# Optimization experiments

Hardware: AMD Instinct MI355X
Metric: run time of the kernel (lower is better)

## Reference

```python
import jax, jax.numpy as jnp
import numpy as np

N_NODES = 100000
N_EDGES = 1000000
D = 64
N_LAYERS = 3
BATCH = 4096


def setup_inputs() -> dict:
    key = jax.random.key(0)
    ks = jax.random.split(key, 12)
    inp = {
        "embeds": jax.random.normal(ks[0], (N_NODES, D), dtype=jnp.float32) * 0.1,
        "edge_weight": jax.random.uniform(ks[1], (N_EDGES,), dtype=jnp.float32),
        "W_gc": jax.random.normal(ks[2], (N_LAYERS, D, D), dtype=jnp.float32) * 0.1,
        "b_gc": jax.random.normal(ks[3], (N_LAYERS, 1, D), dtype=jnp.float32) * 0.1,
        "W_bi": jax.random.normal(ks[4], (N_LAYERS, D, D), dtype=jnp.float32) * 0.1,
        "b_bi": jax.random.normal(ks[5], (N_LAYERS, 1, D), dtype=jnp.float32) * 0.1,
        "edge_index": jax.random.randint(ks[6], (2, N_EDGES), 0, N_NODES, dtype=jnp.int64) if jax.config.jax_enable_x64 else jax.random.randint(ks[6], (2, N_EDGES), 0, N_NODES, dtype=jnp.int32),
        "users": jax.random.randint(ks[7], (BATCH,), 0, 50000, dtype=jnp.int32),
        "pos_items": jax.random.randint(ks[8], (BATCH,), 0, N_NODES, dtype=jnp.int32),
        "neg_items": jax.random.randint(ks[9], (BATCH,), 0, N_NODES, dtype=jnp.int32),
    }
    return inp


def _l2_normalize(x, eps=1e-12):
    # matches torch F.normalize(p=2, dim=1): divide by clamped norm
    n = jnp.sqrt(jnp.sum(x * x, axis=1, keepdims=True))
    return x / jnp.maximum(n, eps)


def reference(embeds, edge_weight, W_gc, b_gc, W_bi, b_bi, edge_index, users, pos_items, neg_items):
    row, col = edge_index[0], edge_index[1]
    n_nodes = embeds.shape[0]
    ego = embeds
    all_embeddings = [ego]
    for k in range(W_gc.shape[0]):
        # gather-scale-scatter graph aggregation
        msgs = ego[row] * edge_weight[:, None]                     # [E, D]
        side = jax.ops.segment_sum(msgs, col, num_segments=n_nodes)  # [N, D]
        sum_emb = side @ W_gc[k] + b_gc[k]                          # [N, D]
        bi_emb = (ego * side) @ W_bi[k] + b_bi[k]                   # [N, D]
        ego = jax.nn.leaky_relu(sum_emb + bi_emb, negative_slope=0.2)
        all_embeddings.append(_l2_normalize(ego))
    all_embeddings = jnp.concatenate(all_embeddings, axis=1)        # [N, 4*D]
    user_embs = all_embeddings[users]
    pos_item_embs = all_embeddings[pos_items]
    neg_item_embs = all_embeddings[neg_items]
    return (user_embs, pos_item_embs, neg_item_embs, user_embs, pos_item_embs, neg_item_embs)
```

## Files before the change

kernel.cpp:

```cpp
#include <hip/hip_runtime.h>

#define NN 100000
#define NE 1000000
#define DD 64
#define NB 4096
#define TILE 1024
#define NTILE ((NN + TILE - 1) / TILE)

__global__ __launch_bounds__(256) void k_count(
    const int* __restrict__ ei, int* __restrict__ base)
{
  const int stride = gridDim.x * blockDim.x;
  for (int e = blockIdx.x * blockDim.x + threadIdx.x; e < NE; e += stride)
    atomicAdd(&base[ei[NE + e]], 1);
}

__global__ __launch_bounds__(256) void k_scan_part(
    const int* __restrict__ base, int* __restrict__ tilesum)
{
  __shared__ int s[256];
  const int t = threadIdx.x;
  const int i0 = blockIdx.x * TILE + t * 4;
  int4 v = make_int4(0, 0, 0, 0);
  if (i0 < NN) v = *reinterpret_cast<const int4*>(base + i0);
  s[t] = v.x + v.y + v.z + v.w;
  __syncthreads();
#pragma unroll
  for (int off = 128; off >= 1; off >>= 1) {
    if (t < off) s[t] += s[t + off];
    __syncthreads();
  }
  if (t == 0) tilesum[blockIdx.x] = s[0];
}

__global__ __launch_bounds__(128) void k_scan_tiles(
    const int* __restrict__ tilesum, int* __restrict__ tileoff)
{
  __shared__ int s[128];
  const int t = threadIdx.x;
  const int v = (t < NTILE) ? tilesum[t] : 0;
  s[t] = v;
  __syncthreads();
#pragma unroll
  for (int off = 1; off < 128; off <<= 1) {
    const int u = (t >= off) ? s[t - off] : 0;
    __syncthreads();
    s[t] += u;
    __syncthreads();
  }
  if (t < NTILE) tileoff[t] = s[t] - v;
}

__global__ __launch_bounds__(256) void k_scan_apply(
    int* __restrict__ base, int* __restrict__ cursor,
    const int* __restrict__ tileoff)
{
  __shared__ int s[256];
  const int t = threadIdx.x;
  const int i0 = blockIdx.x * TILE + t * 4;
  int4 v = make_int4(0, 0, 0, 0);
  if (i0 < NN) v = *reinterpret_cast<const int4*>(base + i0);
  const int sum = v.x + v.y + v.z + v.w;
  s[t] = sum;
  __syncthreads();
#pragma unroll
  for (int off = 1; off < 256; off <<= 1) {
    const int u = (t >= off) ? s[t - off] : 0;
    __syncthreads();
    s[t] += u;
    __syncthreads();
  }
  int p = s[t] - sum + tileoff[blockIdx.x];
  if (i0 < NN) {
    const int4 o = make_int4(p, p + v.x, p + v.x + v.y, p + v.x + v.y + v.z);
    *reinterpret_cast<int4*>(base + i0) = o;
    *reinterpret_cast<int4*>(cursor + i0) = o;
  }
  if (blockIdx.x == 0 && t == 0) base[NN] = NE;
}

__global__ __launch_bounds__(256) void k_permute(
    const int* __restrict__ ei, const float* __restrict__ ew,
    int* __restrict__ cursor, int2* __restrict__ edata)
{
  const int stride = gridDim.x * blockDim.x;
  for (int e = blockIdx.x * blockDim.x + threadIdx.x; e < NE; e += stride) {
    const int c = ei[NE + e];
    const int slot = atomicAdd(&cursor[c], 1);
    edata[slot] = make_int2(ei[e], __float_as_int(ew[e]));
  }
}

__global__ __launch_bounds__(256) void k_aggregate(
    const float* __restrict__ ego, const int* __restrict__ base,
    const int2* __restrict__ edata, float* __restrict__ side)
{
  const int lane = threadIdx.x & 63;
  const int gw = (blockIdx.x * 256 + threadIdx.x) >> 6;
  const int nw = (gridDim.x * 256) >> 6;
  for (int n = gw; n < NN; n += nw) {
    const int lo = base[n];
    const int hi = base[n + 1];
    float acc = 0.f;
    int j = lo;
    for (; j + 1 < hi; j += 2) {
      const int2 a = edata[j];
      const int2 b = edata[j + 1];
      const float va = ego[(size_t)a.x * DD + lane];
      const float vb = ego[(size_t)b.x * DD + lane];
      acc = fmaf(va, __int_as_float(a.y), acc);
      acc = fmaf(vb, __int_as_float(b.y), acc);
    }
    if (j < hi) {
      const int2 a = edata[j];
      acc = fmaf(ego[(size_t)a.x * DD + lane], __int_as_float(a.y), acc);
    }
    side[(size_t)n * DD + lane] = acc;
  }
}

__global__ __launch_bounds__(256) void k_update(
    const float* __restrict__ side, const float* __restrict__ ego_in,
    float* __restrict__ ego_out, float* __restrict__ normed,
    const float* __restrict__ Wgc, const float* __restrict__ bgc,
    const float* __restrict__ Wbi, const float* __restrict__ bbi)
{
  const int lane = threadIdx.x & 63;
  float wg[DD], wb[DD];
#pragma unroll
  for (int j = 0; j < DD; ++j) {
    wg[j] = Wgc[j * DD + lane];
    wb[j] = Wbi[j * DD + lane];
  }
  const float bias = bgc[lane] + bbi[lane];
  const int gw = (blockIdx.x * 256 + threadIdx.x) >> 6;
  const int nw = (gridDim.x * 256) >> 6;
  for (int n = gw; n < NN; n += nw) {
    const float s = side[(size_t)n * DD + lane];
    const float e = ego_in[(size_t)n * DD + lane];
    const float p = s * e;
    float ag = 0.f, ab = 0.f;
#pragma unroll
    for (int j = 0; j < DD; ++j) {
      const float sj = __uint_as_float(__builtin_amdgcn_readlane(__float_as_uint(s), j));
      const float pj = __uint_as_float(__builtin_amdgcn_readlane(__float_as_uint(p), j));
      ag = fmaf(sj, wg[j], ag);
      ab = fmaf(pj, wb[j], ab);
    }
    float x = ag + ab + bias;
    x = (x > 0.f) ? x : 0.2f * x;
    ego_out[(size_t)n * DD + lane] = x;
    float ss = x * x;
#pragma unroll
    for (int off = 32; off >= 1; off >>= 1) ss += __shfl_xor(ss, off);
    const float nrm = fmaxf(sqrtf(ss), 1e-12f);
    normed[(size_t)n * DD + lane] = x / nrm;
  }
}

__global__ __launch_bounds__(256) void k_gather(
    const float* __restrict__ src, const int* __restrict__ users,
    const int* __restrict__ pos, const int* __restrict__ neg,
    float* __restrict__ out, int colOff)
{
  const int w = (blockIdx.x * 256 + threadIdx.x) >> 6;
  const int lane = threadIdx.x & 63;
  if (w >= 3 * NB) return;
  const int t = w / NB;
  const int i = w - t * NB;
  const int* idxp = (t == 0) ? users : ((t == 1) ? pos : neg);
  const int idx = idxp[i];
  const float v = src[(size_t)idx * DD + lane];
  const size_t o = (size_t)w * 256 + colOff + lane;
  out[o] = v;
  out[o + (size_t)3 * NB * 256] = v;
}

extern "C" void kernel_launch(void* const* d_in, const int* in_sizes, int n_in,
                              void* d_out, int out_size, void* d_ws, size_t ws_size,
                              hipStream_t stream)
{
  const float* embeds = (const float*)d_in[0];
  const float* ew     = (const float*)d_in[1];
  const float* Wgc    = (const float*)d_in[2];
  const float* bgc    = (const float*)d_in[3];
  const float* Wbi    = (const float*)d_in[4];
  const float* bbi    = (const float*)d_in[5];
  const int*   ei     = (const int*)d_in[6];
  const int*   users  = (const int*)d_in[7];
  const int*   pos    = (const int*)d_in[8];
  const int*   neg    = (const int*)d_in[9];
  float* out = (float*)d_out;

  float* side = (float*)d_ws;
  float* ego  = side + (size_t)NN * DD;
  float* norm = ego  + (size_t)NN * DD;
  int*   base   = (int*)(norm + (size_t)NN * DD);
  int*   cursor = base + (NN + 4);
  int*   tiles  = cursor + NN;
  int2*  edata  = (int2*)(tiles + 2 * ((NTILE + 1) & ~1));

  const dim3 blk(256);

  k_gather<<<dim3((3 * NB) / 4), blk, 0, stream>>>(embeds, users, pos, neg, out, 0);

  hipMemsetAsync(base, 0, (size_t)(NN + 4) * sizeof(int), stream);
  k_count<<<dim3(1024), blk, 0, stream>>>(ei, base);
  k_scan_part<<<dim3(NTILE), blk, 0, stream>>>(base, tiles);
  k_scan_tiles<<<dim3(1), dim3(128), 0, stream>>>(tiles, tiles + ((NTILE + 1) & ~1));
  k_scan_apply<<<dim3(NTILE), blk, 0, stream>>>(base, cursor, tiles + ((NTILE + 1) & ~1));
  k_permute<<<dim3(1024), blk, 0, stream>>>(ei, ew, cursor, edata);

  const float* cur = embeds;
  for (int k = 0; k < 3; ++k) {
    k_aggregate<<<dim3(4096), blk, 0, stream>>>(cur, base, edata, side);
    k_update<<<dim3(1024), blk, 0, stream>>>(
        side, cur, ego, norm,
        Wgc + (size_t)k * DD * DD, bgc + (size_t)k * DD,
        Wbi + (size_t)k * DD * DD, bbi + (size_t)k * DD);
    k_gather<<<dim3((3 * NB) / 4), blk, 0, stream>>>(norm, users, pos, neg, out,
                                                     DD * (k + 1));
    cur = ego;
  }
}
```

Baseline: 603.9 us.

## Record per-edge rank during counting to drop second atomic pass; unroll aggregation

The count kernel now saves the atomicAdd return value as each edge's rank within its destination node. The permute kernel then computes the slot as base plus rank instead of doing a second atomic on a cursor array, and the cursor array is removed. The rank buffer reuses the side workspace. The aggregate gather loop is unrolled by four to keep more loads in flight, and the grid sizes for count, permute and update are enlarged. The cost is an extra 4MB write and read of ranks in exchange for one fewer contended atomic per edge.

```diff
diff --git a/kernel.cpp b/kernel.cpp
--- a/kernel.cpp
+++ b/kernel.cpp
@@ -8,11 +8,11 @@
 #define NTILE ((NN + TILE - 1) / TILE)
 
 __global__ __launch_bounds__(256) void k_count(
-    const int* __restrict__ ei, int* __restrict__ base)
+    const int* __restrict__ ei, int* __restrict__ base, int* __restrict__ rank)
 {
   const int stride = gridDim.x * blockDim.x;
   for (int e = blockIdx.x * blockDim.x + threadIdx.x; e < NE; e += stride)
-    atomicAdd(&base[ei[NE + e]], 1);
+    rank[e] = atomicAdd(&base[ei[NE + e]], 1);
 }
 
 __global__ __launch_bounds__(256) void k_scan_part(
@@ -52,8 +52,7 @@
 }
 
 __global__ __launch_bounds__(256) void k_scan_apply(
-    int* __restrict__ base, int* __restrict__ cursor,
-    const int* __restrict__ tileoff)
+    int* __restrict__ base, const int* __restrict__ tileoff)
 {
   __shared__ int s[256];
   const int t = threadIdx.x;
@@ -74,19 +73,19 @@
   if (i0 < NN) {
     const int4 o = make_int4(p, p + v.x, p + v.x + v.y, p + v.x + v.y + v.z);
     *reinterpret_cast<int4*>(base + i0) = o;
-    *reinterpret_cast<int4*>(cursor + i0) = o;
   }
   if (blockIdx.x == 0 && t == 0) base[NN] = NE;
 }
 
 __global__ __launch_bounds__(256) void k_permute(
     const int* __restrict__ ei, const float* __restrict__ ew,
-    int* __restrict__ cursor, int2* __restrict__ edata)
+    const int* __restrict__ base, const int* __restrict__ rank,
+    int2* __restrict__ edata)
 {
   const int stride = gridDim.x * blockDim.x;
   for (int e = blockIdx.x * blockDim.x + threadIdx.x; e < NE; e += stride) {
     const int c = ei[NE + e];
-    const int slot = atomicAdd(&cursor[c], 1);
+    const int slot = base[c] + rank[e];
     edata[slot] = make_int2(ei[e], __float_as_int(ew[e]));
   }
 }
@@ -103,15 +102,21 @@
     const int hi = base[n + 1];
     float acc = 0.f;
     int j = lo;
-    for (; j + 1 < hi; j += 2) {
+    for (; j + 3 < hi; j += 4) {
       const int2 a = edata[j];
       const int2 b = edata[j + 1];
+      const int2 c = edata[j + 2];
+      const int2 d = edata[j + 3];
       const float va = ego[(size_t)a.x * DD + lane];
       const float vb = ego[(size_t)b.x * DD + lane];
+      const float vc = ego[(size_t)c.x * DD + lane];
+      const float vd = ego[(size_t)d.x * DD + lane];
       acc = fmaf(va, __int_as_float(a.y), acc);
       acc = fmaf(vb, __int_as_float(b.y), acc);
+      acc = fmaf(vc, __int_as_float(c.y), acc);
+      acc = fmaf(vd, __int_as_float(d.y), acc);
     }
-    if (j < hi) {
+    for (; j < hi; ++j) {
       const int2 a = edata[j];
       acc = fmaf(ego[(size_t)a.x * DD + lane], __int_as_float(a.y), acc);
     }
@@ -196,25 +201,25 @@
   float* ego  = side + (size_t)NN * DD;
   float* norm = ego  + (size_t)NN * DD;
   int*   base   = (int*)(norm + (size_t)NN * DD);
-  int*   cursor = base + (NN + 4);
-  int*   tiles  = cursor + NN;
+  int*   tiles  = base + (NN + 4);
   int2*  edata  = (int2*)(tiles + 2 * ((NTILE + 1) & ~1));
+  int*   rank = (int*)side;
 
   const dim3 blk(256);
 
   k_gather<<<dim3((3 * NB) / 4), blk, 0, stream>>>(embeds, users, pos, neg, out, 0);
 
   hipMemsetAsync(base, 0, (size_t)(NN + 4) * sizeof(int), stream);
-  k_count<<<dim3(1024), blk, 0, stream>>>(ei, base);
+  k_count<<<dim3(4096), blk, 0, stream>>>(ei, base, rank);
   k_scan_part<<<dim3(NTILE), blk, 0, stream>>>(base, tiles);
   k_scan_tiles<<<dim3(1), dim3(128), 0, stream>>>(tiles, tiles + ((NTILE + 1) & ~1));
-  k_scan_apply<<<dim3(NTILE), blk, 0, stream>>>(base, cursor, tiles + ((NTILE + 1) & ~1));
-  k_permute<<<dim3(1024), blk, 0, stream>>>(ei, ew, cursor, edata);
+  k_scan_apply<<<dim3(NTILE), blk, 0, stream>>>(base, tiles + ((NTILE + 1) & ~1));
+  k_permute<<<dim3(4096), blk, 0, stream>>>(ei, ew, base, rank, edata);
 
   const float* cur = embeds;
   for (int k = 0; k < 3; ++k) {
     k_aggregate<<<dim3(4096), blk, 0, stream>>>(cur, base, edata, side);
-    k_update<<<dim3(1024), blk, 0, stream>>>(
+    k_update<<<dim3(2048), blk, 0, stream>>>(
         side, cur, ego, norm,
         Wgc + (size_t)k * DD * DD, bgc + (size_t)k * DD,
         Wbi + (size_t)k * DD * DD, bbi + (size_t)k * DD);
```

Result: faster. 489.9 us (-18.9%).
